# Kernel optimization log

Measured on AMD Instinct MI355X. Metric: run time of the kernel, lower is better.

## Reference

```python
import jax, jax.numpy as jnp
import numpy as np

N_NODES = 50000
N_EDGES = 800000
IN_DIM = 256
EMB_DIM = 256
N_COMS = 4
D_COM = EMB_DIM // N_COMS  # 64
BN_EPS = 1e-5


def setup_inputs() -> dict:
    key = jax.random.key(0)
    ks = jax.random.split(key, 16)
    s1 = 1.0 / np.sqrt(IN_DIM)
    s2 = 1.0 / np.sqrt(D_COM)
    return {
        "x": jax.random.normal(ks[0], (N_NODES, IN_DIM), jnp.float32),
        "edge_index": jax.random.randint(ks[1], (2, N_EDGES), 0, N_NODES, jnp.int32),
        "ew": jax.random.uniform(ks[2], (N_COMS, N_EDGES), jnp.float32),
        "W1_0": jax.random.normal(ks[3], (N_COMS, IN_DIM, D_COM), jnp.float32) * s1,
        "b1_0": jnp.zeros((N_COMS, D_COM), jnp.float32),
        "W2_0": jax.random.normal(ks[4], (N_COMS, D_COM, D_COM), jnp.float32) * s2,
        "b2_0": jnp.zeros((N_COMS, D_COM), jnp.float32),
        "g0": jnp.ones((N_COMS, D_COM), jnp.float32),
        "bt0": jnp.zeros((N_COMS, D_COM), jnp.float32),
        "W1_1": jax.random.normal(ks[5], (N_COMS, D_COM, D_COM), jnp.float32) * s2,
        "b1_1": jnp.zeros((N_COMS, D_COM), jnp.float32),
        "W2_1": jax.random.normal(ks[6], (N_COMS, D_COM, D_COM), jnp.float32) * s2,
        "b2_1": jnp.zeros((N_COMS, D_COM), jnp.float32),
        "g1": jnp.ones((N_COMS, D_COM), jnp.float32),
        "bt1": jnp.zeros((N_COMS, D_COM), jnp.float32),
        "encW": jax.random.normal(ks[7], (IN_DIM, EMB_DIM), jnp.float32) * s1,
        "encb": jnp.zeros((EMB_DIM,), jnp.float32),
    }


def _gin_bn_relu(h, src, dst, w, W1, b1, W2, b2, gamma, beta):
    # weighted scatter-add aggregation: agg[i] = sum_{e:(j->i)} w_e * h[j]
    msg = h[src] * w[:, None]                       # [E, F]
    agg = jax.ops.segment_sum(msg, dst, num_segments=N_NODES)
    z = h + agg                                      # eps = 0 (train_eps=False)
    z = jax.nn.relu(z @ W1 + b1) @ W2 + b2           # GIN MLP
    mu = jnp.mean(z, axis=0)
    var = jnp.var(z, axis=0)
    z = gamma * (z - mu) * jax.lax.rsqrt(var + BN_EPS) + beta
    return jax.nn.relu(z)                            # dropout: eval mode no-op


def reference(x, edge_index, ew, W1_0, b1_0, W2_0, b2_0, g0, bt0,
              W1_1, b1_1, W2_1, b2_1, g1, bt1, encW, encb):
    src, dst = edge_index[0], edge_index[1]
    outs1, outs2 = [], []
    for k in range(N_COMS):
        h1 = _gin_bn_relu(x, src, dst, ew[k], W1_0[k], b1_0[k], W2_0[k], b2_0[k], g0[k], bt0[k])
        h2 = _gin_bn_relu(h1, src, dst, ew[k], W1_1[k], b1_1[k], W2_1[k], b2_1[k], g1[k], bt1[k])
        outs1.append(h1)
        outs2.append(h2)
    out1 = jnp.concatenate(outs1, axis=-1)  # [N, emb_dim]
    out2 = jnp.concatenate(outs2, axis=-1)  # [N, emb_dim]
    enc = x @ encW + encb                   # input_encoder
    return (enc, out1, out2)
```

## Files before the change

kernel.cpp:

```cpp
#include <hip/hip_runtime.h>

#define NN 50000
#define NE 800000
#define FDIM 256
#define SCAN_BLOCKS 196

typedef __attribute__((ext_vector_type(8))) short short8v;
typedef __attribute__((ext_vector_type(4))) float float4v;

__device__ __forceinline__ unsigned short f2bf(float f) {
  unsigned u = __float_as_uint(f);
  unsigned r = (u + 0x7fffu + ((u >> 16) & 1u)) >> 16;
  return (unsigned short)r;
}
__device__ __forceinline__ float bf2f(unsigned short b) {
  return __uint_as_float(((unsigned)b) << 16);
}


__global__ __launch_bounds__(256) void k_hist(const int* __restrict__ dst, int* __restrict__ deg) {
  int e = blockIdx.x * 256 + threadIdx.x;
  if (e < NE) atomicAdd(&deg[dst[e]], 1);
}

__device__ __forceinline__ int block_incl_scan(int v, int* wsum) {
  const int tid = threadIdx.x;
  const int lane = tid & 63;
  const int w = tid >> 6;
  int incl = v;
  #pragma unroll
  for (int off = 1; off < 64; off <<= 1) {
    int tmp = __shfl_up(incl, off, 64);
    if (lane >= off) incl += tmp;
  }
  if (lane == 63) wsum[w] = incl;
  __syncthreads();
  int woff = 0;
  #pragma unroll
  for (int k = 0; k < 3; k++)
    if (k < w) woff += wsum[k];
  return woff + incl;
}

__global__ __launch_bounds__(256) void k_scan_a(const int* __restrict__ deg, int* __restrict__ partial) {
  __shared__ int wsum[4];
  int i = blockIdx.x * 256 + threadIdx.x;
  int v = (i < NN) ? deg[i] : 0;
  int incl = block_incl_scan(v, wsum);
  if (threadIdx.x == 255) partial[blockIdx.x] = incl;
}

__global__ __launch_bounds__(256) void k_scan_b(int* __restrict__ partial, int* __restrict__ offs) {
  __shared__ int wsum[4];
  int tid = threadIdx.x;
  int v = (tid < SCAN_BLOCKS) ? partial[tid] : 0;
  int incl = block_incl_scan(v, wsum);
  if (tid < SCAN_BLOCKS) partial[tid] = incl - v;
  if (tid == 255) offs[NN] = incl;
}

__global__ __launch_bounds__(256) void k_scan_c(const int* __restrict__ deg, const int* __restrict__ partial,
                                                int* __restrict__ offs, int* __restrict__ fillp) {
  __shared__ int wsum[4];
  int i = blockIdx.x * 256 + threadIdx.x;
  int v = (i < NN) ? deg[i] : 0;
  int incl = block_incl_scan(v, wsum);
  int excl = partial[blockIdx.x] + incl - v;
  if (i < NN) {
    offs[i] = excl;
    fillp[i] = excl;
  }
}

__global__ __launch_bounds__(256) void k_fillrec(const int* __restrict__ src, const int* __restrict__ dstA,
                                                 const float* __restrict__ ew, int* __restrict__ fillp,
                                                 int4* __restrict__ recs) {
  int e = blockIdx.x * 256 + threadIdx.x;
  if (e < NE) {
    int d = dstA[e];
    int s = src[e];
    unsigned p01 = (unsigned)f2bf(ew[e]) | ((unsigned)f2bf(ew[NE + e]) << 16);
    unsigned p23 = (unsigned)f2bf(ew[2 * NE + e]) | ((unsigned)f2bf(ew[3 * NE + e]) << 16);
    int pos = atomicAdd(&fillp[d], 1);
    recs[pos] = make_int4(s, (int)p01, (int)p23, 0);
  }
}

__global__ __launch_bounds__(256) void k_wprep(const float* __restrict__ W1_0, const float* __restrict__ encW,
                                               const float* __restrict__ W1_1, const float* __restrict__ W2_0,
                                               const float* __restrict__ W2_1, unsigned short* __restrict__ Bt1,
                                               unsigned short* __restrict__ BtE, unsigned short* __restrict__ Wb11,
                                               unsigned short* __restrict__ Wb20, unsigned short* __restrict__ Wb21) {
  const int t = blockIdx.x;
  const int k = threadIdx.x;
  const int c = t >> 6, j = t & 63;
  Bt1[t * 256 + k] = f2bf(W1_0[c * 16384 + k * 64 + j]);
  BtE[t * 256 + k] = f2bf(encW[k * 256 + t]);
  if (k < 64) {
    Wb11[c * 4096 + j * 64 + k] = f2bf(W1_1[c * 4096 + k * 64 + j]);
    Wb20[c * 4096 + j * 64 + k] = f2bf(W2_0[c * 4096 + k * 64 + j]);
    Wb21[c * 4096 + j * 64 + k] = f2bf(W2_1[c * 4096 + k * 64 + j]);
  }
}

__global__ __launch_bounds__(512) void k_mm_fused(const float* __restrict__ x,
                                                  const unsigned short* __restrict__ Bt1,
                                                  const unsigned short* __restrict__ BtE,
                                                  const float* __restrict__ encb,
                                                  unsigned short* __restrict__ Pout,
                                                  float* __restrict__ encout) {
  __shared__ __align__(16) unsigned short xs[64][264];
  const int tid = threadIdx.x;
  const int lane = tid & 63;
  const int w = tid >> 6;
  const int isE = w >> 2;
  const int colw = (w & 3) * 64;
  const int row0 = blockIdx.x * 64;
  const int lr = lane & 15;
  const int lk = (lane >> 4) * 8;

  #pragma unroll
  for (int it = 0; it < 8; it++) {
    int idx = it * 512 + tid;
    int row = idx >> 6;
    int col4 = (idx & 63) * 4;
    int grow = row0 + row;
    if (grow >= NN) grow = NN - 1;
    float4 v = *reinterpret_cast<const float4*>(x + (size_t)grow * 256 + col4);
    ushort4 o;
    o.x = f2bf(v.x); o.y = f2bf(v.y); o.z = f2bf(v.z); o.w = f2bf(v.w);
    *reinterpret_cast<ushort4*>(&xs[row][col4]) = o;
  }
  __syncthreads();

  const unsigned short* Bt = isE ? BtE : Bt1;
  const unsigned short* Bptr[4];
  #pragma unroll
  for (int ct = 0; ct < 4; ct++) Bptr[ct] = Bt + (size_t)(colw + ct * 16 + lr) * 256 + lk;

  float4v acc[4][4];
  #pragma unroll
  for (int rt = 0; rt < 4; rt++)
    #pragma unroll
    for (int ct = 0; ct < 4; ct++) acc[rt][ct] = (float4v){0.f, 0.f, 0.f, 0.f};

  #pragma unroll
  for (int ks = 0; ks < 256; ks += 32) {
    short8v a[4], b[4];
    #pragma unroll
    for (int rt = 0; rt < 4; rt++)
      a[rt] = *reinterpret_cast<const short8v*>(&xs[rt * 16 + lr][ks + lk]);
    #pragma unroll
    for (int ct = 0; ct < 4; ct++) b[ct] = *reinterpret_cast<const short8v*>(Bptr[ct] + ks);
    #pragma unroll
    for (int rt = 0; rt < 4; rt++)
      #pragma unroll
      for (int ct = 0; ct < 4; ct++)
        acc[rt][ct] = __builtin_amdgcn_mfma_f32_16x16x32_bf16(a[rt], b[ct], acc[rt][ct], 0, 0, 0);
  }

  #pragma unroll
  for (int rt = 0; rt < 4; rt++) {
    #pragma unroll
    for (int ct = 0; ct < 4; ct++) {
      const int col = colw + ct * 16 + lr;
      const float bv = isE ? encb[col] : 0.f;
      #pragma unroll
      for (int r = 0; r < 4; r++) {
        const int row = row0 + rt * 16 + (lane >> 4) * 4 + r;
        if (row < NN) {
          float v = acc[rt][ct][r] + bv;
          if (isE)
            encout[(size_t)row * 256 + col] = v;
          else
            Pout[(size_t)row * 256 + col] = f2bf(v);
        }
      }
    }
  }
}

__global__ __launch_bounds__(256) void k_agg(const unsigned short* __restrict__ P,
                                             const int* __restrict__ offs, const int4* __restrict__ recs,
                                             const float* __restrict__ b1, unsigned short* __restrict__ Rb) {
  const int lane = threadIdx.x & 63;
  const int wid = threadIdx.x >> 6;
  const int i = blockIdx.x * 4 + wid;
  const int half = lane >> 5;
  const int l32 = lane & 31;
  const int col0 = l32 * 8;
  const int c = l32 >> 3;

  const int es = offs[i], ee = offs[i + 1];
  float acc[8];
  #pragma unroll
  for (int j = 0; j < 8; j++) acc[j] = 0.f;

  for (int base = es; base < ee; base += 16) {
    int sq[8];
    float wq[8];
    #pragma unroll
    for (int q = 0; q < 8; q++) {
      int e = base + 2 * q + half;
      bool valid = e < ee;
      int4 rv = recs[valid ? e : es];
      sq[q] = rv.x;
      unsigned p = (c < 2) ? (unsigned)rv.y : (unsigned)rv.z;
      unsigned short wb = (c & 1) ? (unsigned short)(p >> 16) : (unsigned short)(p & 0xffff);
      wq[q] = valid ? bf2f(wb) : 0.f;
    }
    short8v pq[8];
    #pragma unroll
    for (int q = 0; q < 8; q++)
      pq[q] = *reinterpret_cast<const short8v*>(P + (size_t)sq[q] * 256 + col0);
    #pragma unroll
    for (int q = 0; q < 8; q++)
      #pragma unroll
      for (int j = 0; j < 8; j++)
        acc[j] = fmaf(wq[q], bf2f((unsigned short)pq[q][j]), acc[j]);
  }

  #pragma unroll
  for (int j = 0; j < 8; j++) acc[j] += __shfl_xor(acc[j], 32);

  if (half == 0) {
    short8v ps = *reinterpret_cast<const short8v*>(P + (size_t)i * 256 + col0);
    float4 b4a = *reinterpret_cast<const float4*>(b1 + col0);
    float4 b4b = *reinterpret_cast<const float4*>(b1 + col0 + 4);
    float bb[8] = {b4a.x, b4a.y, b4a.z, b4a.w, b4b.x, b4b.y, b4b.z, b4b.w};
    short8v out;
    #pragma unroll
    for (int j = 0; j < 8; j++) {
      float r = bf2f((unsigned short)ps[j]) + acc[j] + bb[j];
      out[j] = (short)f2bf(r > 0.f ? r : 0.f);
    }
    *reinterpret_cast<short8v*>(Rb + (size_t)i * 256 + col0) = out;
  }
}

__global__ __launch_bounds__(256) void k_bd_stats(const unsigned short* __restrict__ A,
                                                  const unsigned short* __restrict__ Wz,
                                                  float* __restrict__ bnsum, float* __restrict__ bnsq) {
  const int lane = threadIdx.x & 63;
  const int c = threadIdx.x >> 6;
  const int row0 = blockIdx.x * 64;
  const int lr = lane & 15;
  const int lk = (lane >> 4) * 8;

  const unsigned short* Aptr[4];
  #pragma unroll
  for (int rt = 0; rt < 4; rt++) {
    int row = row0 + rt * 16 + lr;
    if (row >= NN) row = NN - 1;
    Aptr[rt] = A + (size_t)row * 256 + c * 64 + lk;
  }

  float4v acc[4][4];
  #pragma unroll
  for (int rt = 0; rt < 4; rt++)
    #pragma unroll
    for (int ct = 0; ct < 4; ct++) acc[rt][ct] = (float4v){0.f, 0.f, 0.f, 0.f};

  #pragma unroll
  for (int ks = 0; ks < 64; ks += 32) {
    short8v a[4], b[4];
    #pragma unroll
    for (int rt = 0; rt < 4; rt++) a[rt] = *reinterpret_cast<const short8v*>(Aptr[rt] + ks);
    #pragma unroll
    for (int ct = 0; ct < 4; ct++)
      b[ct] = *reinterpret_cast<const short8v*>(Wz + (size_t)c * 4096 + (ct * 16 + lr) * 64 + ks + lk);
    #pragma unroll
    for (int rt = 0; rt < 4; rt++)
      #pragma unroll
      for (int ct = 0; ct < 4; ct++)
        acc[rt][ct] = __builtin_amdgcn_mfma_f32_16x16x32_bf16(a[rt], b[ct], acc[rt][ct], 0, 0, 0);
  }

  #pragma unroll
  for (int ct = 0; ct < 4; ct++) {
    const int col = c * 64 + ct * 16 + lr;
    float s1 = 0.f, s2 = 0.f;
    #pragma unroll
    for (int rt = 0; rt < 4; rt++) {
      #pragma unroll
      for (int r = 0; r < 4; r++) {
        const int row = row0 + rt * 16 + (lane >> 4) * 4 + r;
        if (row < NN) {
          float v = acc[rt][ct][r];
          s1 += v;
          s2 += v * v;
        }
      }
    }
    s1 += __shfl_xor(s1, 16); s1 += __shfl_xor(s1, 32);
    s2 += __shfl_xor(s2, 16); s2 += __shfl_xor(s2, 32);
    if (lane < 16) {
      atomicAdd(&bnsum[col], s1);
      atomicAdd(&bnsq[col], s2);
    }
  }
}

template <int WITH_P2>
__global__ __launch_bounds__(256) void k_bd_bn(const unsigned short* __restrict__ A,
                                               const unsigned short* __restrict__ Wz,
                                               const float* __restrict__ bnsum, const float* __restrict__ bnsq,
                                               const float* __restrict__ g, const float* __restrict__ bt,
                                               const unsigned short* __restrict__ Wp,
                                               float* __restrict__ Hout, unsigned short* __restrict__ P2out) {
  __shared__ __align__(16) unsigned short h_lds[64][264];
  const int lane = threadIdx.x & 63;
  const int c = threadIdx.x >> 6;
  const int row0 = blockIdx.x * 64;
  const int lr = lane & 15;
  const int lk = (lane >> 4) * 8;
  const int rbase = (lane >> 4) * 4;

  const unsigned short* Aptr[4];
  #pragma unroll
  for (int rt = 0; rt < 4; rt++) {
    int row = row0 + rt * 16 + lr;
    if (row >= NN) row = NN - 1;
    Aptr[rt] = A + (size_t)row * 256 + c * 64 + lk;
  }

  float4v acc[4][4];
  #pragma unroll
  for (int rt = 0; rt < 4; rt++)
    #pragma unroll
    for (int ct = 0; ct < 4; ct++) acc[rt][ct] = (float4v){0.f, 0.f, 0.f, 0.f};

  #pragma unroll
  for (int ks = 0; ks < 64; ks += 32) {
    short8v a[4], b[4];
    #pragma unroll
    for (int rt = 0; rt < 4; rt++) a[rt] = *reinterpret_cast<const short8v*>(Aptr[rt] + ks);
    #pragma unroll
    for (int ct = 0; ct < 4; ct++)
      b[ct] = *reinterpret_cast<const short8v*>(Wz + (size_t)c * 4096 + (ct * 16 + lr) * 64 + ks + lk);
    #pragma unroll
    for (int rt = 0; rt < 4; rt++)
      #pragma unroll
      for (int ct = 0; ct < 4; ct++)
        acc[rt][ct] = __builtin_amdgcn_mfma_f32_16x16x32_bf16(a[rt], b[ct], acc[rt][ct], 0, 0, 0);
  }

  float sc[4], sh[4];
  #pragma unroll
  for (int ct = 0; ct < 4; ct++) {
    const int t = c * 64 + ct * 16 + lr;
    float mu = bnsum[t] * (1.f / NN);
    float var = bnsq[t] * (1.f / NN) - mu * mu;
    var = var > 0.f ? var : 0.f;
    float rs = rsqrtf(var + 1e-5f);
    sc[ct] = g[t] * rs;
    sh[ct] = bt[t] - mu * sc[ct];
  }

  #pragma unroll
  for (int rt = 0; rt < 4; rt++) {
    #pragma unroll
    for (int ct = 0; ct < 4; ct++) {
      const int col = c * 64 + ct * 16 + lr;
      #pragma unroll
      for (int r = 0; r < 4; r++) {
        const int rowl = rt * 16 + rbase + r;
        const int row = row0 + rowl;
        float h = fmaf(acc[rt][ct][r], sc[ct], sh[ct]);
        h = h > 0.f ? h : 0.f;
        if (row < NN) Hout[(size_t)row * 256 + col] = h;
        if (WITH_P2) h_lds[rowl][col] = f2bf(h);
      }
    }
  }

  if (WITH_P2) {
    __syncthreads();
    float4v acc2[4][4];
    #pragma unroll
    for (int rt = 0; rt < 4; rt++)
      #pragma unroll
      for (int ct = 0; ct < 4; ct++) acc2[rt][ct] = (float4v){0.f, 0.f, 0.f, 0.f};
    #pragma unroll
    for (int ks = 0; ks < 64; ks += 32) {
      short8v a[4], b[4];
      #pragma unroll
      for (int rt = 0; rt < 4; rt++)
        a[rt] = *reinterpret_cast<const short8v*>(&h_lds[rt * 16 + lr][c * 64 + ks + lk]);
      #pragma unroll
      for (int ct = 0; ct < 4; ct++)
        b[ct] = *reinterpret_cast<const short8v*>(Wp + (size_t)c * 4096 + (ct * 16 + lr) * 64 + ks + lk);
      #pragma unroll
      for (int rt = 0; rt < 4; rt++)
        #pragma unroll
        for (int ct = 0; ct < 4; ct++)
          acc2[rt][ct] = __builtin_amdgcn_mfma_f32_16x16x32_bf16(a[rt], b[ct], acc2[rt][ct], 0, 0, 0);
    }
    #pragma unroll
    for (int rt = 0; rt < 4; rt++) {
      #pragma unroll
      for (int ct = 0; ct < 4; ct++) {
        const int col = c * 64 + ct * 16 + lr;
        #pragma unroll
        for (int r = 0; r < 4; r++) {
          const int row = row0 + rt * 16 + rbase + r;
          if (row < NN) P2out[(size_t)row * 256 + col] = f2bf(acc2[rt][ct][r]);
        }
      }
    }
  }
}


extern "C" void kernel_launch(void* const* d_in, const int* in_sizes, int n_in,
                              void* d_out, int out_size, void* d_ws, size_t ws_size,
                              hipStream_t stream) {
  const float* x    = (const float*)d_in[0];
  const int*   ei   = (const int*)d_in[1];
  const float* ew   = (const float*)d_in[2];
  const float* W1_0 = (const float*)d_in[3];
  const float* b1_0 = (const float*)d_in[4];
  const float* W2_0 = (const float*)d_in[5];
  const float* g0   = (const float*)d_in[7];
  const float* bt0  = (const float*)d_in[8];
  const float* W1_1 = (const float*)d_in[9];
  const float* b1_1 = (const float*)d_in[10];
  const float* W2_1 = (const float*)d_in[11];
  const float* g1   = (const float*)d_in[13];
  const float* bt1  = (const float*)d_in[14];
  const float* encW = (const float*)d_in[15];
  const float* encb = (const float*)d_in[16];

  const int* srcA = ei;
  const int* dstA = ei + NE;

  float* out_enc = (float*)d_out;
  float* out1 = out_enc + (size_t)NN * FDIM;
  float* out2 = out1 + (size_t)NN * FDIM;

  unsigned short* P1bf = (unsigned short*)out1;
  unsigned short* P2bf = (unsigned short*)out2;

  char* wp = (char*)d_ws;
  auto carve = [&](size_t bytes) {
    char* r = wp;
    wp += (bytes + 255) & ~(size_t)255;
    return r;
  };
  int*   deg     = (int*)carve((size_t)NN * 4);
  int*   offs    = (int*)carve((size_t)(NN + 1) * 4);
  int*   fillp   = (int*)carve((size_t)NN * 4);
  int*   partial = (int*)carve(SCAN_BLOCKS * 4);
  float* bnsum0  = (float*)carve(256 * 4);
  float* bnsq0   = (float*)carve(256 * 4);
  float* bnsum1  = (float*)carve(256 * 4);
  float* bnsq1   = (float*)carve(256 * 4);
  unsigned short* Bt1  = (unsigned short*)carve(256 * 256 * 2);
  unsigned short* BtE  = (unsigned short*)carve(256 * 256 * 2);
  unsigned short* Wb11 = (unsigned short*)carve(4 * 64 * 64 * 2);
  unsigned short* Wb20 = (unsigned short*)carve(4 * 64 * 64 * 2);
  unsigned short* Wb21 = (unsigned short*)carve(4 * 64 * 64 * 2);
  int4* recs           = (int4*)carve((size_t)NE * 16);
  unsigned short* Rb   = (unsigned short*)carve((size_t)NN * FDIM * 2);

  hipMemsetAsync(deg, 0, (size_t)NN * 4, stream);
  hipMemsetAsync(bnsum0, 0, 4 * 1024, stream);

  k_hist<<<(NE + 255) / 256, 256, 0, stream>>>(dstA, deg);
  k_scan_a<<<SCAN_BLOCKS, 256, 0, stream>>>(deg, partial);
  k_scan_b<<<1, 256, 0, stream>>>(partial, offs);
  k_scan_c<<<SCAN_BLOCKS, 256, 0, stream>>>(deg, partial, offs, fillp);
  k_fillrec<<<(NE + 255) / 256, 256, 0, stream>>>(srcA, dstA, ew, fillp, recs);

  k_wprep<<<256, 256, 0, stream>>>(W1_0, encW, W1_1, W2_0, W2_1, Bt1, BtE, Wb11, Wb20, Wb21);

  const int MMG = (NN + 63) / 64;

  k_mm_fused<<<MMG, 512, 0, stream>>>(x, Bt1, BtE, encb, P1bf, out_enc);

  k_agg<<<NN / 4, 256, 0, stream>>>(P1bf, offs, recs, b1_0, Rb);
  k_bd_stats<<<MMG, 256, 0, stream>>>(Rb, Wb20, bnsum0, bnsq0);
  k_bd_bn<1><<<MMG, 256, 0, stream>>>(Rb, Wb20, bnsum0, bnsq0, g0, bt0, Wb11, out1, P2bf);

  k_agg<<<NN / 4, 256, 0, stream>>>(P2bf, offs, recs, b1_1, Rb);
  k_bd_stats<<<MMG, 256, 0, stream>>>(Rb, Wb21, bnsum1, bnsq1);
  k_bd_bn<0><<<MMG, 256, 0, stream>>>(Rb, Wb21, bnsum1, bnsq1, g1, bt1, nullptr, out2, nullptr);
}
```

Before: 388.7 us.

## Split fused GEMM across grid, stage outputs through LDS, merge wprep into scan

```diff
diff --git a/kernel.cpp b/kernel.cpp
--- a/kernel.cpp
+++ b/kernel.cpp
@@ -50,13 +50,31 @@
   if (threadIdx.x == 255) partial[blockIdx.x] = incl;
 }
 
-__global__ __launch_bounds__(256) void k_scan_b(int* __restrict__ partial, int* __restrict__ offs) {
-  __shared__ int wsum[4];
-  int tid = threadIdx.x;
-  int v = (tid < SCAN_BLOCKS) ? partial[tid] : 0;
-  int incl = block_incl_scan(v, wsum);
-  if (tid < SCAN_BLOCKS) partial[tid] = incl - v;
-  if (tid == 255) offs[NN] = incl;
+__global__ __launch_bounds__(256) void k_scanb_wprep(int* __restrict__ partial, int* __restrict__ offs,
+                                                     const float* __restrict__ W1_0, const float* __restrict__ encW,
+                                                     const float* __restrict__ W1_1, const float* __restrict__ W2_0,
+                                                     const float* __restrict__ W2_1, unsigned short* __restrict__ Bt1,
+                                                     unsigned short* __restrict__ BtE, unsigned short* __restrict__ Wb11,
+                                                     unsigned short* __restrict__ Wb20, unsigned short* __restrict__ Wb21) {
+  if (blockIdx.x == 256) {
+    __shared__ int wsum[4];
+    int tid = threadIdx.x;
+    int v = (tid < SCAN_BLOCKS) ? partial[tid] : 0;
+    int incl = block_incl_scan(v, wsum);
+    if (tid < SCAN_BLOCKS) partial[tid] = incl - v;
+    if (tid == 255) offs[NN] = incl;
+    return;
+  }
+  const int t = blockIdx.x;
+  const int k = threadIdx.x;
+  const int c = t >> 6, j = t & 63;
+  Bt1[t * 256 + k] = f2bf(W1_0[c * 16384 + k * 64 + j]);
+  BtE[t * 256 + k] = f2bf(encW[k * 256 + t]);
+  if (k < 64) {
+    Wb11[c * 4096 + j * 64 + k] = f2bf(W1_1[c * 4096 + k * 64 + j]);
+    Wb20[c * 4096 + j * 64 + k] = f2bf(W2_0[c * 4096 + k * 64 + j]);
+    Wb21[c * 4096 + j * 64 + k] = f2bf(W2_1[c * 4096 + k * 64 + j]);
+  }
 }
 
 __global__ __launch_bounds__(256) void k_scan_c(const int* __restrict__ deg, const int* __restrict__ partial,
@@ -86,42 +104,35 @@
   }
 }
 
-__global__ __launch_bounds__(256) void k_wprep(const float* __restrict__ W1_0, const float* __restrict__ encW,
-                                               const float* __restrict__ W1_1, const float* __restrict__ W2_0,
-                                               const float* __restrict__ W2_1, unsigned short* __restrict__ Bt1,
-                                               unsigned short* __restrict__ BtE, unsigned short* __restrict__ Wb11,
-                                               unsigned short* __restrict__ Wb20, unsigned short* __restrict__ Wb21) {
-  const int t = blockIdx.x;
-  const int k = threadIdx.x;
-  const int c = t >> 6, j = t & 63;
-  Bt1[t * 256 + k] = f2bf(W1_0[c * 16384 + k * 64 + j]);
-  BtE[t * 256 + k] = f2bf(encW[k * 256 + t]);
-  if (k < 64) {
-    Wb11[c * 4096 + j * 64 + k] = f2bf(W1_1[c * 4096 + k * 64 + j]);
-    Wb20[c * 4096 + j * 64 + k] = f2bf(W2_0[c * 4096 + k * 64 + j]);
-    Wb21[c * 4096 + j * 64 + k] = f2bf(W2_1[c * 4096 + k * 64 + j]);
-  }
-}
-
-__global__ __launch_bounds__(512) void k_mm_fused(const float* __restrict__ x,
-                                                  const unsigned short* __restrict__ Bt1,
-                                                  const unsigned short* __restrict__ BtE,
-                                                  const float* __restrict__ encb,
-                                                  unsigned short* __restrict__ Pout,
-                                                  float* __restrict__ encout) {
+__global__ __launch_bounds__(256, 4) void k_mm_fused(const float* __restrict__ x,
+                                                     const unsigned short* __restrict__ Bt1,
+                                                     const unsigned short* __restrict__ BtE,
+                                                     const float* __restrict__ encb,
+                                                     unsigned short* __restrict__ Pout,
+                                                     float* __restrict__ encout) {
   __shared__ __align__(16) unsigned short xs[64][264];
   const int tid = threadIdx.x;
   const int lane = tid & 63;
   const int w = tid >> 6;
-  const int isE = w >> 2;
-  const int colw = (w & 3) * 64;
+  const int isE = blockIdx.y;
+  const int colw = w * 64;
   const int row0 = blockIdx.x * 64;
   const int lr = lane & 15;
   const int lk = (lane >> 4) * 8;
-
-  #pragma unroll
-  for (int it = 0; it < 8; it++) {
-    int idx = it * 512 + tid;
+  const int rbase = (lane >> 4) * 4;
+
+  const unsigned short* Bt = isE ? BtE : Bt1;
+  const unsigned short* Bptr[4];
+  #pragma unroll
+  for (int ct = 0; ct < 4; ct++) Bptr[ct] = Bt + (size_t)(colw + ct * 16 + lr) * 256 + lk;
+
+  short8v bcur[4];
+  #pragma unroll
+  for (int ct = 0; ct < 4; ct++) bcur[ct] = *reinterpret_cast<const short8v*>(Bptr[ct]);
+
+  #pragma unroll
+  for (int it = 0; it < 16; it++) {
+    int idx = it * 256 + tid;
     int row = idx >> 6;
     int col4 = (idx & 63) * 4;
     int grow = row0 + row;
@@ -133,11 +144,6 @@
   }
   __syncthreads();
 
-  const unsigned short* Bt = isE ? BtE : Bt1;
-  const unsigned short* Bptr[4];
-  #pragma unroll
-  for (int ct = 0; ct < 4; ct++) Bptr[ct] = Bt + (size_t)(colw + ct * 16 + lr) * 256 + lk;
-
   float4v acc[4][4];
   #pragma unroll
   for (int rt = 0; rt < 4; rt++)
@@ -145,37 +151,76 @@
     for (int ct = 0; ct < 4; ct++) acc[rt][ct] = (float4v){0.f, 0.f, 0.f, 0.f};
 
   #pragma unroll
-  for (int ks = 0; ks < 256; ks += 32) {
-    short8v a[4], b[4];
+  for (int ks8 = 0; ks8 < 8; ks8++) {
+    const int ks = ks8 * 32;
+    short8v bnxt[4];
+    if (ks8 < 7) {
+      #pragma unroll
+      for (int ct = 0; ct < 4; ct++) bnxt[ct] = *reinterpret_cast<const short8v*>(Bptr[ct] + ks + 32);
+    }
+    short8v a[4];
     #pragma unroll
     for (int rt = 0; rt < 4; rt++)
       a[rt] = *reinterpret_cast<const short8v*>(&xs[rt * 16 + lr][ks + lk]);
     #pragma unroll
-    for (int ct = 0; ct < 4; ct++) b[ct] = *reinterpret_cast<const short8v*>(Bptr[ct] + ks);
-    #pragma unroll
     for (int rt = 0; rt < 4; rt++)
       #pragma unroll
       for (int ct = 0; ct < 4; ct++)
-        acc[rt][ct] = __builtin_amdgcn_mfma_f32_16x16x32_bf16(a[rt], b[ct], acc[rt][ct], 0, 0, 0);
-  }
-
-  #pragma unroll
-  for (int rt = 0; rt < 4; rt++) {
-    #pragma unroll
-    for (int ct = 0; ct < 4; ct++) {
-      const int col = colw + ct * 16 + lr;
-      const float bv = isE ? encb[col] : 0.f;
-      #pragma unroll
-      for (int r = 0; r < 4; r++) {
-        const int row = row0 + rt * 16 + (lane >> 4) * 4 + r;
-        if (row < NN) {
-          float v = acc[rt][ct][r] + bv;
-          if (isE)
-            encout[(size_t)row * 256 + col] = v;
-          else
-            Pout[(size_t)row * 256 + col] = f2bf(v);
-        }
+        acc[rt][ct] = __builtin_amdgcn_mfma_f32_16x16x32_bf16(a[rt], bcur[ct], acc[rt][ct], 0, 0, 0);
+    if (ks8 < 7) {
+      #pragma unroll
+      for (int ct = 0; ct < 4; ct++) bcur[ct] = bnxt[ct];
+    }
+  }
+
+  __syncthreads();
+  if (!isE) {
+    #pragma unroll
+    for (int rt = 0; rt < 4; rt++)
+      #pragma unroll
+      for (int ct = 0; ct < 4; ct++) {
+        const int col = colw + ct * 16 + lr;
+        #pragma unroll
+        for (int r = 0; r < 4; r++) xs[rt * 16 + rbase + r][col] = f2bf(acc[rt][ct][r]);
       }
+    __syncthreads();
+    #pragma unroll
+    for (int it = 0; it < 8; it++) {
+      int idx = it * 256 + tid;
+      int row = idx >> 5;
+      int p = idx & 31;
+      if (row0 + row < NN)
+        *reinterpret_cast<short8v*>(Pout + (size_t)(row0 + row) * 256 + p * 8) =
+            *reinterpret_cast<const short8v*>(&xs[row][p * 8]);
+    }
+  } else {
+    float bv[4];
+    #pragma unroll
+    for (int ct = 0; ct < 4; ct++) bv[ct] = encb[colw + ct * 16 + lr];
+    float (*cs)[132] = reinterpret_cast<float(*)[132]>(&xs[0][0]);
+    #pragma unroll
+    for (int ph = 0; ph < 2; ph++) {
+      if ((colw >> 7) == ph) {
+        #pragma unroll
+        for (int rt = 0; rt < 4; rt++)
+          #pragma unroll
+          for (int ct = 0; ct < 4; ct++) {
+            const int col = colw + ct * 16 + lr - ph * 128;
+            #pragma unroll
+            for (int r = 0; r < 4; r++) cs[rt * 16 + rbase + r][col] = acc[rt][ct][r] + bv[ct];
+          }
+      }
+      __syncthreads();
+      #pragma unroll
+      for (int it = 0; it < 8; it++) {
+        int idx = it * 256 + tid;
+        int row = idx >> 5;
+        int p = idx & 31;
+        if (row0 + row < NN)
+          *reinterpret_cast<float4*>(encout + (size_t)(row0 + row) * 256 + ph * 128 + p * 4) =
+              *reinterpret_cast<const float4*>(&cs[row][p * 4]);
+      }
+      __syncthreads();
     }
   }
 }
@@ -468,15 +513,14 @@
 
   k_hist<<<(NE + 255) / 256, 256, 0, stream>>>(dstA, deg);
   k_scan_a<<<SCAN_BLOCKS, 256, 0, stream>>>(deg, partial);
-  k_scan_b<<<1, 256, 0, stream>>>(partial, offs);
+  k_scanb_wprep<<<257, 256, 0, stream>>>(partial, offs, W1_0, encW, W1_1, W2_0, W2_1,
+                                         Bt1, BtE, Wb11, Wb20, Wb21);
   k_scan_c<<<SCAN_BLOCKS, 256, 0, stream>>>(deg, partial, offs, fillp);
   k_fillrec<<<(NE + 255) / 256, 256, 0, stream>>>(srcA, dstA, ew, fillp, recs);
 
-  k_wprep<<<256, 256, 0, stream>>>(W1_0, encW, W1_1, W2_0, W2_1, Bt1, BtE, Wb11, Wb20, Wb21);
-
   const int MMG = (NN + 63) / 64;
 
-  k_mm_fused<<<MMG, 512, 0, stream>>>(x, Bt1, BtE, encb, P1bf, out_enc);
+  k_mm_fused<<<dim3(MMG, 2), 256, 0, stream>>>(x, Bt1, BtE, encb, P1bf, out_enc);
 
   k_agg<<<NN / 4, 256, 0, stream>>>(P1bf, offs, recs, b1_0, Rb);
   k_bd_stats<<<MMG, 256, 0, stream>>>(Rb, Wb20, bnsum0, bnsq0);
```

After: 384.1 us. Within noise of the previous version (-1.2%).
